# Kernel optimization log

Hardware: AMD Instinct MI355X
Metric: run time of the kernel (lower is better)

The kernel has to match this reference:

```python
import math
import jax, jax.numpy as jnp
import numpy as np

B, S, D, H, FF, E, V, RH = 8, 256, 512, 8, 2048, 8, 32000, 256
MAX_PATH, MAX_VISITS = 4, 2
NEG = -1e9
DH = D // H


def _make_pe():
    # PositionalEncoding buffer (sin/cos), sliced to seq len S
    pos = np.arange(S, dtype=np.float32)[:, None]
    div = np.exp(np.arange(0, D, 2, dtype=np.float32) * (-math.log(10000.0) / D))
    pe = np.zeros((S, D), dtype=np.float32)
    pe[:, 0::2] = np.sin(pos * div)
    pe[:, 1::2] = np.cos(pos * div)
    return jnp.asarray(pe[None])  # [1,S,D]


def setup_inputs() -> dict:
    key = jax.random.key(0)
    ks = jax.random.split(key, 12)
    s = 0.02
    return dict(
        input_ids=jax.random.randint(ks[0], (B, S), 0, V),
        emb=jax.random.normal(ks[1], (V, D), jnp.float32) * s,
        pe=_make_pe(),
        Wqkv=jax.random.normal(ks[2], (E, 3 * D, D), jnp.float32) * s,
        bqkv=jnp.zeros((E, 3 * D), jnp.float32),
        Wo=jax.random.normal(ks[3], (E, D, D), jnp.float32) * s,
        bo=jnp.zeros((E, D), jnp.float32),
        W1=jax.random.normal(ks[4], (E, FF, D), jnp.float32) * s,
        b1=jnp.zeros((E, FF), jnp.float32),
        W2=jax.random.normal(ks[5], (E, D, FF), jnp.float32) * s,
        b2=jnp.zeros((E, D), jnp.float32),
        ln1_g=jnp.ones((E, D), jnp.float32), ln1_b=jnp.zeros((E, D), jnp.float32),
        ln2_g=jnp.ones((E, D), jnp.float32), ln2_b=jnp.zeros((E, D), jnp.float32),
        tag=jax.random.normal(ks[6], (E, D), jnp.float32) * 0.01,
        r_w1=jax.random.normal(ks[7], (RH, D), jnp.float32) * s,
        r_b1=jnp.zeros((RH,), jnp.float32),
        r_w2=jax.random.normal(ks[8], (E + 1, RH), jnp.float32) * s,
        r_b2=jnp.zeros((E + 1,), jnp.float32),
        lm_w=jax.random.normal(ks[9], (V, D), jnp.float32) * s,
        lm_b=jnp.zeros((V,), jnp.float32),
    )


def _ln(x, g, b):
    # per-sample gathered LayerNorm params g,b: [B,D]; x: [B,S,D]
    mu = x.mean(-1, keepdims=True)
    var = ((x - mu) ** 2).mean(-1, keepdims=True)
    return (x - mu) * jax.lax.rsqrt(var + 1e-5) * g[:, None, :] + b[:, None, :]


def _expert(x, idx, Wqkv, bqkv, Wo, bo, W1, b1, W2, b2, g1, be1, g2, be2, tag):
    # post-norm TransformerEncoderLayer (eval mode, dropout off) with per-sample expert params
    qkv = jnp.einsum('bsd,bfd->bsf', x, Wqkv[idx]) + bqkv[idx][:, None, :]
    q, k, v = jnp.split(qkv, 3, axis=-1)
    q = q.reshape(B, S, H, DH)
    k = k.reshape(B, S, H, DH)
    v = v.reshape(B, S, H, DH)
    att = jax.nn.softmax(jnp.einsum('bqhd,bkhd->bhqk', q, k) / math.sqrt(DH), axis=-1)
    ctx = jnp.einsum('bhqk,bkhd->bqhd', att, v).reshape(B, S, D)
    attn_out = jnp.einsum('bsd,bod->bso', ctx, Wo[idx]) + bo[idx][:, None, :]
    x = _ln(x + attn_out, g1[idx], be1[idx])
    hid = jax.nn.relu(jnp.einsum('bsd,bfd->bsf', x, W1[idx]) + b1[idx][:, None, :])
    ff = jnp.einsum('bsf,bdf->bsd', hid, W2[idx]) + b2[idx][:, None, :]
    x = _ln(x + ff, g2[idx], be2[idx])
    return x + tag[idx][:, None, :]  # + specialization_tag


def reference(input_ids, emb, pe, Wqkv, bqkv, Wo, bo, W1, b1, W2, b2,
              ln1_g, ln1_b, ln2_g, ln2_b, tag, r_w1, r_b1, r_w2, r_b2, lm_w, lm_b):
    pad_mask = (jnp.arange(V) != 0).astype(emb.dtype)[:, None]  # padding_idx=0 row is zero
    rep = (emb * pad_mask)[input_ids] * math.sqrt(D) + pe[:, :S]
    visits = jnp.zeros((B, E), jnp.int32)
    active = jnp.ones((B,), bool)
    ent_total = jnp.asarray(0.0, rep.dtype)
    for _ in range(MAX_PATH):
        summary = rep.mean(1)  # [B,D]
        h = jax.nn.relu(summary @ r_w1.T + r_b1)
        logits = h @ r_w2.T + r_b2  # [B,E+1], last slot = terminate
        logits = jnp.concatenate(
            [jnp.where(visits >= MAX_VISITS, NEG, logits[:, :E]), logits[:, E:]], axis=1)
        probs = jax.nn.softmax(logits, axis=-1)
        ent = -jnp.sum(probs * jnp.log(probs + 1e-9), axis=-1)
        cnt = jnp.sum(active)
        ent_total = ent_total + jnp.where(
            cnt > 0, jnp.sum(ent * active) / jnp.maximum(cnt, 1).astype(ent.dtype), 0.0)
        choice = jnp.argmax(logits, axis=-1)       # eval mode: hard argmax
        go = active & (choice < E)                 # samples routed to an expert this step
        idx = jnp.where(go, choice, 0)
        visits = visits + jax.nn.one_hot(idx, E, dtype=jnp.int32) * go[:, None].astype(jnp.int32)
        new_rep = _expert(rep, idx, Wqkv, bqkv, Wo, bo, W1, b1, W2, b2,
                          ln1_g, ln1_b, ln2_g, ln2_b, tag)
        rep = jnp.where(go[:, None, None], new_rep, rep)  # terminated/inactive reps frozen
        active = go
    logits_lm = rep @ lm_w.T + lm_b  # [B,S,V]
    return logits_lm, ent_total
```

## Files before the change

kernel.cpp:

```cpp
#include <hip/hip_runtime.h>
#include <hip/hip_bf16.h>

#define NB 8
#define NS 256
#define ND 512
#define NH 8
#define NDH 64
#define NFF 2048
#define NE 8
#define NV 32000
#define NRH 256
#define MAXV 2
#define NEGV (-1e9f)

typedef __attribute__((ext_vector_type(8))) short short8;
typedef __attribute__((ext_vector_type(4))) float f32x4;

__device__ __forceinline__ unsigned short f2bf(float x) {
  unsigned int u = __float_as_uint(x);
  u = (u + 0x7fffu + ((u >> 16) & 1u)) >> 16;
  return (unsigned short)u;
}
__device__ __forceinline__ float bf2f(unsigned short x) {
  return __uint_as_float(((unsigned int)x) << 16);
}

__device__ __forceinline__ void gload16(const unsigned short* g, unsigned short* l) {
  __builtin_amdgcn_global_load_lds(
      (const __attribute__((address_space(1))) unsigned int*)g,
      (__attribute__((address_space(3))) unsigned int*)l, 16, 0, 0);
}

__device__ __forceinline__ int swzc(int lane) {
  return (lane & 3) ^ ((lane >> 3) & 3);
}

__device__ __forceinline__ void cast8(const float* s, unsigned short* d, int j) {
  const float4* s4 = (const float4*)s;
  float4 a = s4[j * 2], b = s4[j * 2 + 1];
  short8 v;
  v[0] = (short)f2bf(a.x); v[1] = (short)f2bf(a.y);
  v[2] = (short)f2bf(a.z); v[3] = (short)f2bf(a.w);
  v[4] = (short)f2bf(b.x); v[5] = (short)f2bf(b.y);
  v[6] = (short)f2bf(b.z); v[7] = (short)f2bf(b.w);
  *(short8*)&d[(size_t)j * 8] = v;
}

__global__ __launch_bounds__(256) void k_cast5e(
    const float* s0, unsigned short* d0, int n0,
    const float* s1, unsigned short* d1, int n1,
    const float* s2, unsigned short* d2, int n2,
    const float* s3, unsigned short* d3, int n3,
    const float* s4, unsigned short* d4, int n4,
    int nbcast,
    const int* __restrict__ ids, const float* __restrict__ emb,
    const float* __restrict__ pe,
    unsigned short* __restrict__ repb, float* __restrict__ partial,
    int* visits, int* active, float* entp) {
  if (blockIdx.x == 0) {
    if (threadIdx.x < NB * NE) visits[threadIdx.x] = 0;
    if (threadIdx.x < NB) active[threadIdx.x] = 1;
    if (threadIdx.x == 0) *entp = 0.f;
  }
  if ((int)blockIdx.x >= nbcast) {
    int j2 = blockIdx.x - nbcast;
    int rg = j2 & 15, b = j2 >> 4;
    int t = threadIdx.x;
    int c0 = t, c1 = t + 256;
    float pa0 = 0.f, pa1 = 0.f, pb0 = 0.f, pb1 = 0.f;
    for (int row = 0; row < 16; ++row) {
      int s = rg * 16 + row;
      int id = ids[b * NS + s];
      float sc = (id != 0) ? 22.627416997969522f : 0.f;
      float v0 = emb[(size_t)id * ND + c0] * sc + pe[(size_t)s * ND + c0];
      float v1 = emb[(size_t)id * ND + c1] * sc + pe[(size_t)s * ND + c1];
      size_t base = ((size_t)b * NS + s) * ND;
      repb[base + c0] = f2bf(v0); repb[base + c1] = f2bf(v1);
      if (row < 8) { pa0 += v0; pa1 += v1; } else { pb0 += v0; pb1 += v1; }
    }
    float* ppa = partial + ((size_t)b * 32 + rg * 2) * ND;
    float* ppb = ppa + ND;
    ppa[c0] = pa0; ppa[c1] = pa1;
    ppb[c0] = pb0; ppb[c1] = pb1;
    return;
  }
  int j = blockIdx.x * 256 + threadIdx.x;
  if (j < n0) { cast8(s0, d0, j); return; }
  j -= n0;
  if (j < n1) { cast8(s1, d1, j); return; }
  j -= n1;
  if (j < n2) { cast8(s2, d2, j); return; }
  j -= n2;
  if (j < n3) { cast8(s3, d3, j); return; }
  j -= n3;
  if (j < n4) cast8(s4, d4, j);
}

__global__ __launch_bounds__(256) void k_router8(
    const float* __restrict__ partial,
    const float* __restrict__ rw1, const float* __restrict__ rb1,
    const float* __restrict__ rw2, const float* __restrict__ rb2,
    int* visits, const int* __restrict__ active_in, int* active_out,
    int* idx, int* go, float* ent_total) {
  int b = blockIdx.x;
  __shared__ float sm[ND];
  __shared__ float h[NRH];
  __shared__ float lg[NE + 1];
  __shared__ int scnt;
  int t = threadIdx.x;
  for (int i = t; i < ND; i += 256) {
    const float* pp = partial + ((size_t)b * 32) * ND + i;
    float s = 0.f;
#pragma unroll
    for (int rg = 0; rg < 32; ++rg) s += pp[(size_t)rg * ND];
    sm[i] = s * (1.f / NS);
  }
  if (t == 0) {
    int c = 0;
    for (int bb = 0; bb < NB; ++bb) c += active_in[bb];
    scnt = c;
  }
  __syncthreads();
  {
    const float* w = rw1 + (size_t)t * ND;
    float acc = rb1[t];
    for (int d = 0; d < ND; ++d) acc += sm[d] * w[d];
    h[t] = fmaxf(acc, 0.f);
  }
  __syncthreads();
  if (t < NE + 1) {
    const float* w = rw2 + t * NRH;
    float a = rb2[t];
    for (int r = 0; r < NRH; ++r) a += h[r] * w[r];
    lg[t] = a;
  }
  __syncthreads();
  if (t == 0) {
    int aprev = active_in[b];
    float l[NE + 1];
    for (int e = 0; e < NE; ++e)
      l[e] = (visits[b * NE + e] >= MAXV) ? NEGV : lg[e];
    l[NE] = lg[NE];
    float m = l[0];
    for (int e = 1; e <= NE; ++e) m = fmaxf(m, l[e]);
    float z = 0.f, p[NE + 1];
    for (int e = 0; e <= NE; ++e) { p[e] = __expf(l[e] - m); z += p[e]; }
    float zi = 1.f / z, ent = 0.f;
    for (int e = 0; e <= NE; ++e) {
      float pp = p[e] * zi;
      ent -= pp * __logf(pp + 1e-9f);
    }
    if (aprev && scnt > 0) atomicAdd(ent_total, ent / (float)scnt);
    int ch = 0; float bm = l[0];
    for (int e = 1; e <= NE; ++e) if (l[e] > bm) { bm = l[e]; ch = e; }
    int g = (aprev && ch < NE) ? 1 : 0;
    int ix = g ? ch : 0;
    visits[b * NE + ix] += g;
    idx[b] = ix; go[b] = g; active_out[b] = g;
  }
}

template <int OUT, int RELU, int SK>
__global__ __launch_bounds__(256) void k_gemm64p(
    const unsigned short* __restrict__ Aall, int sa,
    const unsigned short* __restrict__ Wall, const float* __restrict__ ball,
    float* __restrict__ Pall, unsigned short* __restrict__ Uall, int so,
    int N, int K,
    unsigned short* __restrict__ Qb, unsigned short* __restrict__ Kb,
    unsigned short* __restrict__ Vt,
    const int* __restrict__ go, const int* __restrict__ idx) {
  int b = blockIdx.z;
  if (!go[b]) return;
  int t = threadIdx.x;
  int lane = t & 63, w = t >> 6;
  int wm = (w >> 1) * 32, wn = (w & 1) * 32;
  int kc = blockIdx.x >> 2;
  int bm = (blockIdx.x & 3) * 64, bn = blockIdx.y * 64;
  int KC = K / SK;
  int lrow = (lane >> 4) * 4, lcol = lane & 15;
  const unsigned short* A = Aall + (size_t)b * sa + kc * KC;
  const unsigned short* W = Wall + (size_t)idx[b] * N * K + kc * KC;

  __shared__ __align__(16) unsigned short As[2][64][64];
  __shared__ __align__(16) unsigned short Bs[2][64][64];
  f32x4 acc[2][2];
#pragma unroll
  for (int i = 0; i < 2; ++i)
#pragma unroll
    for (int j = 0; j < 2; ++j) acc[i][j] = (f32x4){0.f, 0.f, 0.f, 0.f};

  int ch8 = (lane & 7) ^ ((lane >> 3) & 7);
  const unsigned short* ga = A + (size_t)(bm + w * 16 + (lane >> 3)) * K + ch8 * 8;
  const unsigned short* gb = W + (size_t)(bn + w * 16 + (lane >> 3)) * K + ch8 * 8;

#define ISSUE64(slot, kt)                                            \
  gload16(ga + (size_t)(kt) * 64, &As[slot][w * 16][0]);             \
  gload16(ga + (size_t)(kt) * 64 + 8 * (size_t)K, &As[slot][w * 16 + 8][0]); \
  gload16(gb + (size_t)(kt) * 64, &Bs[slot][w * 16][0]);             \
  gload16(gb + (size_t)(kt) * 64 + 8 * (size_t)K, &Bs[slot][w * 16 + 8][0]);

  int nk = KC >> 6;
  ISSUE64(0, 0)
  ISSUE64(1, 1)

  int row0 = lane & 15, g = lane >> 4;
  for (int it = 0; it < nk; ++it) {
    if (it < nk - 1) asm volatile("s_waitcnt vmcnt(4)" ::: "memory");
    else             asm volatile("s_waitcnt vmcnt(0)" ::: "memory");
    asm volatile("s_barrier" ::: "memory");
    int sl = it & 1;
    __builtin_amdgcn_s_setprio(1);
#pragma unroll
    for (int kk = 0; kk < 2; ++kk) {
      int co = ((kk * 4 + g) ^ (row0 & 7)) * 8;
      short8 a0 = *(const short8*)&As[sl][wm + row0][co];
      short8 a1 = *(const short8*)&As[sl][wm + 16 + row0][co];
      short8 b0 = *(const short8*)&Bs[sl][wn + row0][co];
      short8 b1 = *(const short8*)&Bs[sl][wn + 16 + row0][co];
      acc[0][0] = __builtin_amdgcn_mfma_f32_16x16x32_bf16(a0, b0, acc[0][0], 0, 0, 0);
      acc[0][1] = __builtin_amdgcn_mfma_f32_16x16x32_bf16(a0, b1, acc[0][1], 0, 0, 0);
      acc[1][0] = __builtin_amdgcn_mfma_f32_16x16x32_bf16(a1, b0, acc[1][0], 0, 0, 0);
      acc[1][1] = __builtin_amdgcn_mfma_f32_16x16x32_bf16(a1, b1, acc[1][1], 0, 0, 0);
    }
    __builtin_amdgcn_s_setprio(0);
    asm volatile("s_barrier" ::: "memory");
    if (it + 2 < nk) { ISSUE64(sl, it + 2) }
  }
#undef ISSUE64

  if (OUT == 2) {
    const float* bias = ball + (size_t)idx[b] * N;
    int seg = bn >> 9;
#pragma unroll
    for (int nf = 0; nf < 2; ++nf) {
      int col = bn + wn + nf * 16 + lcol;
      float bv = bias[col];
      if (seg < 2) {
        unsigned short* dst = (seg == 0) ? Qb : Kb;
        int cc = col - seg * 512;
#pragma unroll
        for (int mf = 0; mf < 2; ++mf)
#pragma unroll
          for (int r = 0; r < 4; ++r) {
            int row = bm + wm + mf * 16 + lrow + r;
            dst[((size_t)b * NS + row) * ND + cc] = f2bf(acc[mf][nf][r] + bv);
          }
      } else {
        int dcol = col - 1024;
#pragma unroll
        for (int mf = 0; mf < 2; ++mf) {
          int s0 = bm + wm + mf * 16 + lrow;
          unsigned long long pk =
              (unsigned long long)f2bf(acc[mf][nf][0] + bv) |
              ((unsigned long long)f2bf(acc[mf][nf][1] + bv) << 16) |
              ((unsigned long long)f2bf(acc[mf][nf][2] + bv) << 32) |
              ((unsigned long long)f2bf(acc[mf][nf][3] + bv) << 48);
          *(unsigned long long*)&Vt[((size_t)b * 512 + dcol) * 256 + s0] = pk;
        }
      }
    }
  } else if (OUT == 1) {
    const float* bias = ball + (size_t)idx[b] * N;
#pragma unroll
    for (int nf = 0; nf < 2; ++nf) {
      int col = bn + wn + nf * 16 + lcol;
      float bv = bias[col];
#pragma unroll
      for (int mf = 0; mf < 2; ++mf) {
#pragma unroll
        for (int r = 0; r < 4; ++r) {
          int row = bm + wm + mf * 16 + lrow + r;
          float v = acc[mf][nf][r] + bv;
          if (RELU) v = fmaxf(v, 0.f);
          Uall[(size_t)b * so + (size_t)row * N + col] = f2bf(v);
        }
      }
    }
  } else {
    float* P = Pall + ((size_t)kc * NB + b) * ((size_t)NS * N);
#pragma unroll
    for (int nf = 0; nf < 2; ++nf) {
      int col = bn + wn + nf * 16 + lcol;
#pragma unroll
      for (int mf = 0; mf < 2; ++mf)
#pragma unroll
        for (int r = 0; r < 4; ++r)
          P[(size_t)(bm + wm + mf * 16 + lrow + r) * N + col] = acc[mf][nf][r];
    }
  }
}

__global__ __launch_bounds__(256) void k_attn2(const unsigned short* __restrict__ Qb,
                                               const unsigned short* __restrict__ Kb,
                                               const unsigned short* __restrict__ Vt,
                                               unsigned short* __restrict__ ctxb,
                                               const int* __restrict__ go) {
  int b = blockIdx.z, h = blockIdx.y, qt = blockIdx.x;
  if (!go[b]) return;
  int t = threadIdx.x;
  __shared__ __align__(16) unsigned short lds0[16384];
  int lane = t & 63, w = t >> 6, g = lane >> 4, c = lane & 15;

#pragma unroll
  for (int i = 0; i < 8; ++i) {
    int task = i * 256 + t;
    int k = task >> 3, cc = task & 7;
    short8 v = *(const short8*)&Kb[((size_t)b * NS + k) * ND + h * NDH + cc * 8];
    *(short8*)&lds0[k * 64 + ((cc * 8) ^ ((k & 7) << 3))] = v;
  }
  short8 qf[2];
  {
    const unsigned short* qp = Qb + ((size_t)b * NS + qt * 64 + w * 16 + c) * ND + h * NDH;
    qf[0] = *(const short8*)&qp[g * 8];
    qf[1] = *(const short8*)&qp[32 + g * 8];
  }
  __syncthreads();

  f32x4 sacc[16];
#pragma unroll
  for (int mf = 0; mf < 16; ++mf) sacc[mf] = (f32x4){0.f, 0.f, 0.f, 0.f};
#pragma unroll
  for (int mf = 0; mf < 16; ++mf) {
#pragma unroll
    for (int kd = 0; kd < 2; ++kd) {
      int row = mf * 16 + c;
      short8 kf = *(const short8*)&lds0[row * 64 + ((kd * 32 + g * 8) ^ ((row & 7) << 3))];
      sacc[mf] = __builtin_amdgcn_mfma_f32_16x16x32_bf16(kf, qf[kd], sacc[mf], 0, 0, 0);
    }
  }
  __syncthreads();

  float mx = -3.4e38f;
#pragma unroll
  for (int mf = 0; mf < 16; ++mf) {
#pragma unroll
    for (int r = 0; r < 4; ++r) {
      sacc[mf][r] *= 0.125f;
      mx = fmaxf(mx, sacc[mf][r]);
    }
  }
  mx = fmaxf(mx, __shfl_xor(mx, 16));
  mx = fmaxf(mx, __shfl_xor(mx, 32));
  float sum = 0.f;
#pragma unroll
  for (int mf = 0; mf < 16; ++mf)
#pragma unroll
    for (int r = 0; r < 4; ++r) {
      float p = __expf(sacc[mf][r] - mx);
      sacc[mf][r] = p;
      sum += p;
    }
  sum += __shfl_xor(sum, 16);
  sum += __shfl_xor(sum, 32);
  float zi = 1.f / sum;

  int q_l = w * 16 + c;
#pragma unroll
  for (int mf = 0; mf < 16; ++mf) {
    unsigned long long pk =
        (unsigned long long)f2bf(sacc[mf][0] * zi) |
        ((unsigned long long)f2bf(sacc[mf][1] * zi) << 16) |
        ((unsigned long long)f2bf(sacc[mf][2] * zi) << 32) |
        ((unsigned long long)f2bf(sacc[mf][3] * zi) << 48);
    *(unsigned long long*)&lds0[q_l * 256 + ((mf * 16 + g * 4) ^ ((q_l & 7) << 3))] = pk;
  }
  __syncthreads();

  f32x4 cacc[4];
#pragma unroll
  for (int nf = 0; nf < 4; ++nf) cacc[nf] = (f32x4){0.f, 0.f, 0.f, 0.f};
  const unsigned short* vbase = Vt + ((size_t)b * 512 + h * NDH) * 256;
#pragma unroll
  for (int ks = 0; ks < 8; ++ks) {
    int prow = w * 16 + c;
    short8 pf = *(const short8*)&lds0[prow * 256 + ((ks * 32 + g * 8) ^ ((prow & 7) << 3))];
#pragma unroll
    for (int nf = 0; nf < 4; ++nf) {
      short8 vf = *(const short8*)&vbase[(size_t)(nf * 16 + c) * 256 + ks * 32 + g * 8];
      cacc[nf] = __builtin_amdgcn_mfma_f32_16x16x32_bf16(pf, vf, cacc[nf], 0, 0, 0);
    }
  }
#pragma unroll
  for (int nf = 0; nf < 4; ++nf)
#pragma unroll
    for (int r = 0; r < 4; ++r)
      ctxb[((size_t)b * NS + qt * 64 + w * 16 + g * 4 + r) * ND + h * NDH + nf * 16 + c] =
          f2bf(cacc[nf][r]);
}

template <int NCH, int TAG, int SUMP>
__global__ __launch_bounds__(256) void k_ln_red(
    const unsigned short* __restrict__ resb, const float* __restrict__ part,
    const float* __restrict__ gbias,
    const float* __restrict__ gall, const float* __restrict__ beall,
    const float* __restrict__ tagall,
    unsigned short* __restrict__ outb,
    float* __restrict__ sump,
    const int* __restrict__ go, const int* __restrict__ idx) {
  int b = blockIdx.y;
  if (!go[b]) return;
  int rg = blockIdx.x;
  int w = threadIdx.x >> 6, l = threadIdx.x & 63;
  int ix = idx[b];
  int d = l * 8;
  float gb8[8], gg[8], bb[8];
  {
    float4 a0 = *(const float4*)&gbias[ix * ND + d];
    float4 a1 = *(const float4*)&gbias[ix * ND + d + 4];
    gb8[0] = a0.x; gb8[1] = a0.y; gb8[2] = a0.z; gb8[3] = a0.w;
    gb8[4] = a1.x; gb8[5] = a1.y; gb8[6] = a1.z; gb8[7] = a1.w;
    float4 g0 = *(const float4*)&gall[ix * ND + d];
    float4 g1 = *(const float4*)&gall[ix * ND + d + 4];
    gg[0] = g0.x; gg[1] = g0.y; gg[2] = g0.z; gg[3] = g0.w;
    gg[4] = g1.x; gg[5] = g1.y; gg[6] = g1.z; gg[7] = g1.w;
    float4 b0 = *(const float4*)&beall[ix * ND + d];
    float4 b1 = *(const float4*)&beall[ix * ND + d + 4];
    bb[0] = b0.x; bb[1] = b0.y; bb[2] = b0.z; bb[3] = b0.w;
    bb[4] = b1.x; bb[5] = b1.y; bb[6] = b1.z; bb[7] = b1.w;
    if (TAG) {
      float4 t0 = *(const float4*)&tagall[ix * ND + d];
      float4 t1 = *(const float4*)&tagall[ix * ND + d + 4];
      bb[0] += t0.x; bb[1] += t0.y; bb[2] += t0.z; bb[3] += t0.w;
      bb[4] += t1.x; bb[5] += t1.y; bb[6] += t1.z; bb[7] += t1.w;
    }
  }
  float ps[8] = {0.f, 0.f, 0.f, 0.f, 0.f, 0.f, 0.f, 0.f};
  const size_t CSTRIDE = (size_t)NB * NS * ND;
  for (int rr = 0; rr < 2; ++rr) {
    int s = rg * 8 + w * 2 + rr;
    size_t base = ((size_t)b * NS + s) * ND;
    short8 xr = *(const short8*)&resb[base + d];
    float v[8];
#pragma unroll
    for (int j = 0; j < 8; ++j) v[j] = bf2f((unsigned short)xr[j]) + gb8[j];
#pragma unroll
    for (int c = 0; c < NCH; ++c) {
      const float* pc = part + c * CSTRIDE + base;
      float4 p0 = *(const float4*)&pc[d];
      float4 p1 = *(const float4*)&pc[d + 4];
      v[0] += p0.x; v[1] += p0.y; v[2] += p0.z; v[3] += p0.w;
      v[4] += p1.x; v[5] += p1.y; v[6] += p1.z; v[7] += p1.w;
    }
    float sum = 0.f;
#pragma unroll
    for (int j = 0; j < 8; ++j) sum += v[j];
#pragma unroll
    for (int off = 1; off < 64; off <<= 1) sum += __shfl_xor(sum, off);
    float mu = sum * (1.f / ND);
    float var = 0.f;
#pragma unroll
    for (int j = 0; j < 8; ++j) { v[j] -= mu; var += v[j] * v[j]; }
#pragma unroll
    for (int off = 1; off < 64; off <<= 1) var += __shfl_xor(var, off);
    float rs = rsqrtf(var * (1.f / ND) + 1e-5f);
    float o[8];
    short8 ob;
#pragma unroll
    for (int j = 0; j < 8; ++j) {
      o[j] = v[j] * rs * gg[j] + bb[j];
      if (SUMP) ps[j] += o[j];
      ob[j] = (short)f2bf(o[j]);
    }
    *(short8*)&outb[base + d] = ob;
  }
  if (SUMP) {
    __shared__ float pl[4][ND];
#pragma unroll
    for (int j = 0; j < 8; ++j) pl[w][d + j] = ps[j];
    __syncthreads();
    if (w == 0) {
      float* pp = sump + ((size_t)b * 32 + rg) * ND;
#pragma unroll
      for (int j = 0; j < 8; ++j)
        pp[d + j] = pl[0][d + j] + pl[1][d + j] + pl[2][d + j] + pl[3][d + j];
    }
  }
}

__global__ __launch_bounds__(512, 2) void k_lmhead256(const unsigned short* __restrict__ Ab,
                                                      const unsigned short* __restrict__ Wb,
                                                      const float* __restrict__ bias,
                                                      float* __restrict__ out,
                                                      const float* __restrict__ entp) {
  if (blockIdx.x == 0 && threadIdx.x == 0)
    out[(size_t)NB * NS * NV] = *entp;
  int id = blockIdx.x;
  int swz = (id & 7) * 125 + (id >> 3);
  int bm = (swz % 8) * 256;
  int bn = (swz / 8) * 256;

  __shared__ __align__(16) unsigned short As[2][256][32];
  __shared__ __align__(16) unsigned short Bs[2][256][32];
  int t = threadIdx.x;
  int lane = t & 63, w = t >> 6;
  int wm = (w >> 2) * 128, wn = (w & 3) * 64;
  f32x4 acc[8][4];
#pragma unroll
  for (int i = 0; i < 8; ++i)
#pragma unroll
    for (int j = 0; j < 4; ++j) acc[i][j] = (f32x4){0.f, 0.f, 0.f, 0.f};

  const unsigned short* ga = Ab + (size_t)(bm + w * 32 + (lane >> 2)) * ND + swzc(lane) * 8;
  const unsigned short* gb = Wb + (size_t)(bn + w * 32 + (lane >> 2)) * ND + swzc(lane) * 8;

#define ISSUEL(slot, kt)                                           \
  gload16(ga + (kt) * 32, &As[slot][w * 32][0]);                   \
  gload16(ga + (kt) * 32 + 16 * ND, &As[slot][w * 32 + 16][0]);    \
  gload16(gb + (kt) * 32, &Bs[slot][w * 32][0]);                   \
  gload16(gb + (kt) * 32 + 16 * ND, &Bs[slot][w * 32 + 16][0]);

  ISSUEL(0, 0)
  ISSUEL(1, 1)

  int row0 = lane & 15;
  int cs = ((lane >> 4) ^ ((row0 >> 1) & 3)) * 8;
  for (int it = 0; it < 16; ++it) {
    if (it < 15) asm volatile("s_waitcnt vmcnt(4)" ::: "memory");
    else         asm volatile("s_waitcnt vmcnt(0)" ::: "memory");
    asm volatile("s_barrier" ::: "memory");
    int sl = it & 1;
    short8 a[8], bfr[4];
#pragma unroll
    for (int mf = 0; mf < 8; ++mf)
      a[mf] = *(const short8*)&As[sl][wm + mf * 16 + row0][cs];
#pragma unroll
    for (int nf = 0; nf < 4; ++nf)
      bfr[nf] = *(const short8*)&Bs[sl][wn + nf * 16 + row0][cs];
    __builtin_amdgcn_s_setprio(1);
#pragma unroll
    for (int mf = 0; mf < 8; ++mf)
#pragma unroll
      for (int nf = 0; nf < 4; ++nf)
        acc[mf][nf] = __builtin_amdgcn_mfma_f32_16x16x32_bf16(a[mf], bfr[nf], acc[mf][nf], 0, 0, 0);
    __builtin_amdgcn_s_setprio(0);
    asm volatile("s_barrier" ::: "memory");
    if (it + 2 < 16) { ISSUEL(sl, it + 2) }
  }
#undef ISSUEL

  int lrow = (lane >> 4) * 4, lcol = lane & 15;
#pragma unroll
  for (int nf = 0; nf < 4; ++nf) {
    int col = bn + wn + nf * 16 + lcol;
    float bv = bias[col];
#pragma unroll
    for (int mf = 0; mf < 8; ++mf) {
#pragma unroll
      for (int r = 0; r < 4; ++r) {
        int row = bm + wm + mf * 16 + lrow + r;
        out[(size_t)row * NV + col] = acc[mf][nf][r] + bv;
      }
    }
  }
}

extern "C" void kernel_launch(void* const* d_in, const int* in_sizes, int n_in,
                              void* d_out, int out_size, void* d_ws, size_t ws_size,
                              hipStream_t stream) {
  const int* ids   = (const int*)d_in[0];
  const float* emb = (const float*)d_in[1];
  const float* pe  = (const float*)d_in[2];
  const float* Wqkv = (const float*)d_in[3];
  const float* bqkv = (const float*)d_in[4];
  const float* Wo   = (const float*)d_in[5];
  const float* bo   = (const float*)d_in[6];
  const float* W1   = (const float*)d_in[7];
  const float* b1   = (const float*)d_in[8];
  const float* W2   = (const float*)d_in[9];
  const float* b2   = (const float*)d_in[10];
  const float* g1   = (const float*)d_in[11];
  const float* be1  = (const float*)d_in[12];
  const float* g2   = (const float*)d_in[13];
  const float* be2  = (const float*)d_in[14];
  const float* tag  = (const float*)d_in[15];
  const float* rw1  = (const float*)d_in[16];
  const float* rb1  = (const float*)d_in[17];
  const float* rw2  = (const float*)d_in[18];
  const float* rb2  = (const float*)d_in[19];
  const float* lmw  = (const float*)d_in[20];
  const float* lmb  = (const float*)d_in[21];
  float* out = (float*)d_out;

  float* ws = (float*)d_ws;
  size_t o = 0;
  float* partk = ws + o; o += (size_t)4 * NB * NS * ND;
  float* partial = ws + o; o += (size_t)NB * 32 * ND;
  int* visits = (int*)(ws + o); o += 1024;
  int* active0 = visits + NB * NE;
  int* active1 = active0 + NB;
  int* idx = active1 + NB;
  int* go = idx + NB;
  float* entp = (float*)(go + NB);

  unsigned short* us = (unsigned short*)(ws + o);
  size_t uo = 0;
  unsigned short* rep_b = us + uo; uo += (size_t)NB * NS * ND;
  unsigned short* x1_b  = us + uo; uo += (size_t)NB * NS * ND;
  unsigned short* ctx_b = us + uo; uo += (size_t)NB * NS * ND;
  unsigned short* Qb    = us + uo; uo += (size_t)NB * NS * ND;
  unsigned short* Kb    = us + uo; uo += (size_t)NB * NS * ND;
  unsigned short* Vt    = us + uo; uo += (size_t)NB * NS * ND;
  unsigned short* hid_b = us + uo; uo += (size_t)NB * NS * NFF;
  unsigned short* Wqkv_b = us + uo; uo += (size_t)NE * 3 * ND * ND;
  unsigned short* Wo_b   = us + uo; uo += (size_t)NE * ND * ND;
  unsigned short* W1_b   = us + uo; uo += (size_t)NE * NFF * ND;
  unsigned short* W2_b   = us + uo; uo += (size_t)NE * ND * NFF;
  unsigned short* lmw_b  = us + uo; uo += (size_t)NV * ND;

  {
    int n0 = NE * 3 * ND * ND / 8, n1 = NE * ND * ND / 8, n2 = NE * NFF * ND / 8,
        n3 = NE * ND * NFF / 8, n4 = NV * ND / 8;
    int nbcast = (n0 + n1 + n2 + n3 + n4) / 256;
    k_cast5e<<<nbcast + 16 * NB, 256, 0, stream>>>(
        Wqkv, Wqkv_b, n0, Wo, Wo_b, n1, W1, W1_b, n2, W2, W2_b, n3, lmw, lmw_b, n4,
        nbcast, ids, emb, pe, rep_b, partial, visits, active0, entp);
  }

  for (int step = 0; step < 4; ++step) {
    int* act_in  = (step & 1) ? active1 : active0;
    int* act_out = (step & 1) ? active0 : active1;
    k_router8<<<NB, 256, 0, stream>>>(partial, rw1, rb1, rw2, rb2,
                                      visits, act_in, act_out, idx, go, entp);
    k_gemm64p<2, 0, 1><<<dim3(4, 24, NB), 256, 0, stream>>>(
        rep_b, NS * ND, Wqkv_b, bqkv, nullptr, nullptr, 0, 3 * ND, ND,
        Qb, Kb, Vt, go, idx);
    k_attn2<<<dim3(4, NH, NB), 256, 0, stream>>>(Qb, Kb, Vt, ctx_b, go);
    k_gemm64p<0, 0, 2><<<dim3(8, 8, NB), 256, 0, stream>>>(
        ctx_b, NS * ND, Wo_b, nullptr, partk, nullptr, 0, ND, ND,
        nullptr, nullptr, nullptr, go, idx);
    k_ln_red<2, 0, 0><<<dim3(32, NB), 256, 0, stream>>>(
        rep_b, partk, bo, g1, be1, nullptr, x1_b, nullptr, go, idx);
    k_gemm64p<1, 1, 1><<<dim3(4, 32, NB), 256, 0, stream>>>(
        x1_b, NS * ND, W1_b, b1, nullptr, hid_b, NS * NFF, NFF, ND,
        nullptr, nullptr, nullptr, go, idx);
    k_gemm64p<0, 0, 4><<<dim3(16, 8, NB), 256, 0, stream>>>(
        hid_b, NS * NFF, W2_b, nullptr, partk, nullptr, 0, ND, NFF,
        nullptr, nullptr, nullptr, go, idx);
    k_ln_red<4, 1, 1><<<dim3(32, NB), 256, 0, stream>>>(
        x1_b, partk, b2, g2, be2, tag, rep_b, partial, go, idx);
  }

  k_lmhead256<<<1000, 512, 0, stream>>>(rep_b, lmw_b, lmb, out, entp);
}
```

Before: 505.2 us.

## Spread LM-head weight cast across per-step expert kernels as tail blocks

The fp32-to-bf16 conversion of the large LM-head weight is removed from the initial cast kernel. It is now split into chunks handled by extra grid blocks appended to the QKV GEMM, attention, output-projection and FFN1 launches in each routing step. The aim is to hide this bandwidth-bound cast behind the expert compute, which often leaves the GPU underused when few samples are active, and to shorten the serial startup kernel. In exchange, the extra blocks compete with the expert kernels for memory bandwidth and compute units, and the kernels carry additional branches and parameters.

```diff
diff --git a/kernel.cpp b/kernel.cpp
--- a/kernel.cpp
+++ b/kernel.cpp
@@ -12,6 +12,7 @@
 #define NRH 256
 #define MAXV 2
 #define NEGV (-1e9f)
+#define CAST_UNITS (NV * ND / 8)
 
 typedef __attribute__((ext_vector_type(8))) short short8;
 typedef __attribute__((ext_vector_type(4))) float f32x4;
@@ -46,12 +47,19 @@
   *(short8*)&d[(size_t)j * 8] = v;
 }
 
-__global__ __launch_bounds__(256) void k_cast5e(
+__device__ __forceinline__ void cast_tail(const float* csrc, unsigned short* cdst,
+                                          int cbase, int ny) {
+  int ext = (((int)blockIdx.y - ny) * (int)gridDim.z + (int)blockIdx.z) * (int)gridDim.x +
+            (int)blockIdx.x;
+  int unit = cbase + ext * 256 + (int)threadIdx.x;
+  if (unit < CAST_UNITS) cast8(csrc, cdst, unit);
+}
+
+__global__ __launch_bounds__(256) void k_cast4e(
     const float* s0, unsigned short* d0, int n0,
     const float* s1, unsigned short* d1, int n1,
     const float* s2, unsigned short* d2, int n2,
     const float* s3, unsigned short* d3, int n3,
-    const float* s4, unsigned short* d4, int n4,
     int nbcast,
     const int* __restrict__ ids, const float* __restrict__ emb,
     const float* __restrict__ pe,
@@ -91,9 +99,7 @@
   j -= n1;
   if (j < n2) { cast8(s2, d2, j); return; }
   j -= n2;
-  if (j < n3) { cast8(s3, d3, j); return; }
-  j -= n3;
-  if (j < n4) cast8(s4, d4, j);
+  if (j < n3) cast8(s3, d3, j);
 }
 
 __global__ __launch_bounds__(256) void k_router8(
@@ -168,7 +174,13 @@
     int N, int K,
     unsigned short* __restrict__ Qb, unsigned short* __restrict__ Kb,
     unsigned short* __restrict__ Vt,
-    const int* __restrict__ go, const int* __restrict__ idx) {
+    const int* __restrict__ go, const int* __restrict__ idx,
+    const float* __restrict__ csrc, unsigned short* __restrict__ cdst,
+    int cbase, int ny) {
+  if ((int)blockIdx.y >= ny) {
+    cast_tail(csrc, cdst, cbase, ny);
+    return;
+  }
   int b = blockIdx.z;
   if (!go[b]) return;
   int t = threadIdx.x;
@@ -294,7 +306,14 @@
                                                const unsigned short* __restrict__ Kb,
                                                const unsigned short* __restrict__ Vt,
                                                unsigned short* __restrict__ ctxb,
-                                               const int* __restrict__ go) {
+                                               const int* __restrict__ go,
+                                               const float* __restrict__ csrc,
+                                               unsigned short* __restrict__ cdst,
+                                               int cbase, int ny) {
+  if ((int)blockIdx.y >= ny) {
+    cast_tail(csrc, cdst, cbase, ny);
+    return;
+  }
   int b = blockIdx.z, h = blockIdx.y, qt = blockIdx.x;
   if (!go[b]) return;
   int t = threadIdx.x;
@@ -609,33 +628,41 @@
 
   {
     int n0 = NE * 3 * ND * ND / 8, n1 = NE * ND * ND / 8, n2 = NE * NFF * ND / 8,
-        n3 = NE * ND * NFF / 8, n4 = NV * ND / 8;
-    int nbcast = (n0 + n1 + n2 + n3 + n4) / 256;
-    k_cast5e<<<nbcast + 16 * NB, 256, 0, stream>>>(
-        Wqkv, Wqkv_b, n0, Wo, Wo_b, n1, W1, W1_b, n2, W2, W2_b, n3, lmw, lmw_b, n4,
+        n3 = NE * ND * NFF / 8;
+    int nbcast = (n0 + n1 + n2 + n3) / 256;
+    k_cast4e<<<nbcast + 16 * NB, 256, 0, stream>>>(
+        Wqkv, Wqkv_b, n0, Wo, Wo_b, n1, W1, W1_b, n2, W2, W2_b, n3,
         nbcast, ids, emb, pe, rep_b, partial, visits, active0, entp);
   }
+
+  int cb = 0;
+  const int CB_STEP = 512 * 256;
 
   for (int step = 0; step < 4; ++step) {
     int* act_in  = (step & 1) ? active1 : active0;
     int* act_out = (step & 1) ? active0 : active1;
     k_router8<<<NB, 256, 0, stream>>>(partial, rw1, rb1, rw2, rb2,
                                       visits, act_in, act_out, idx, go, entp);
-    k_gemm64p<2, 0, 1><<<dim3(4, 24, NB), 256, 0, stream>>>(
+    k_gemm64p<2, 0, 1><<<dim3(4, 24 + 16, NB), 256, 0, stream>>>(
         rep_b, NS * ND, Wqkv_b, bqkv, nullptr, nullptr, 0, 3 * ND, ND,
-        Qb, Kb, Vt, go, idx);
-    k_attn2<<<dim3(4, NH, NB), 256, 0, stream>>>(Qb, Kb, Vt, ctx_b, go);
-    k_gemm64p<0, 0, 2><<<dim3(8, 8, NB), 256, 0, stream>>>(
+        Qb, Kb, Vt, go, idx, lmw, lmw_b, cb, 24);
+    cb += CB_STEP;
+    k_attn2<<<dim3(4, NH + 16, NB), 256, 0, stream>>>(Qb, Kb, Vt, ctx_b, go,
+                                                      lmw, lmw_b, cb, NH);
+    cb += CB_STEP;
+    k_gemm64p<0, 0, 2><<<dim3(8, 8 + 8, NB), 256, 0, stream>>>(
         ctx_b, NS * ND, Wo_b, nullptr, partk, nullptr, 0, ND, ND,
-        nullptr, nullptr, nullptr, go, idx);
+        nullptr, nullptr, nullptr, go, idx, lmw, lmw_b, cb, 8);
+    cb += CB_STEP;
     k_ln_red<2, 0, 0><<<dim3(32, NB), 256, 0, stream>>>(
         rep_b, partk, bo, g1, be1, nullptr, x1_b, nullptr, go, idx);
-    k_gemm64p<1, 1, 1><<<dim3(4, 32, NB), 256, 0, stream>>>(
+    k_gemm64p<1, 1, 1><<<dim3(4, 32 + 16, NB), 256, 0, stream>>>(
         x1_b, NS * ND, W1_b, b1, nullptr, hid_b, NS * NFF, NFF, ND,
-        nullptr, nullptr, nullptr, go, idx);
+        nullptr, nullptr, nullptr, go, idx, lmw, lmw_b, cb, 32);
+    cb += CB_STEP;
     k_gemm64p<0, 0, 4><<<dim3(16, 8, NB), 256, 0, stream>>>(
         hid_b, NS * NFF, W2_b, nullptr, partk, nullptr, 0, ND, NFF,
-        nullptr, nullptr, nullptr, go, idx);
+        nullptr, nullptr, nullptr, go, idx, lmw, lmw_b, 0, 8);
     k_ln_red<4, 1, 1><<<dim3(32, NB), 256, 0, stream>>>(
         x1_b, partk, b2, g2, be2, tag, rep_b, partial, go, idx);
   }
```

After: 505.4 us. About the same (+0.0%).
